# Kernel tuning notes

Hardware: AMD Instinct MI355X
Metric: run time of the kernel (lower is better)

Reference implementation:

```python
import jax, jax.numpy as jnp
import numpy as np

DIM = 1024
ATT_DIM = 1024
BATCH = 16384


def setup_inputs() -> dict:
    key = jax.random.key(0)
    ks = jax.random.split(key, 10)
    inp = {
        "x": jax.random.normal(ks[0], (BATCH, DIM), dtype=jnp.float32),
        "last_x": jax.random.normal(ks[1], (BATCH, DIM), dtype=jnp.float32),
        "last_num": jax.random.normal(ks[2], (BATCH, ATT_DIM), dtype=jnp.float32),
        "last_den": jax.random.uniform(ks[3], (BATCH, ATT_DIM), dtype=jnp.float32) + 1.0,
        # learned parameters
        "mix_k": jnp.full((1, DIM), 0.5, dtype=jnp.float32),
        "mix_v": jnp.full((1, DIM), 0.5, dtype=jnp.float32),
        "mix_r": jnp.full((1, DIM), 0.5, dtype=jnp.float32),
        "decay": jnp.full((1, ATT_DIM), 0.5, dtype=jnp.float32),
        "bonus": jnp.full((1, ATT_DIM), 0.5, dtype=jnp.float32),
        "Wk": jax.random.normal(ks[4], (DIM, ATT_DIM), dtype=jnp.float32) * (DIM ** -0.5),
        "Wv": jax.random.normal(ks[5], (DIM, ATT_DIM), dtype=jnp.float32) * (DIM ** -0.5),
        "Wr": jax.random.normal(ks[6], (DIM, ATT_DIM), dtype=jnp.float32) * (DIM ** -0.5),
        "Wout": jax.random.normal(ks[7], (ATT_DIM, DIM), dtype=jnp.float32) * (ATT_DIM ** -0.5),
    }
    return inp


def reference(x, last_x, last_num, last_den, mix_k, mix_v, mix_r, decay, bonus,
              Wk, Wv, Wr, Wout):
    # interpolated token-shift mixing, then thin projections
    k = (x * mix_k + last_x * (1.0 - mix_k)) @ Wk          # [B, A]
    v = (x * mix_v + last_x * (1.0 - mix_v)) @ Wv          # [B, A]
    r = jax.nn.sigmoid((x * mix_r + last_x * (1.0 - mix_r)) @ Wr)  # [B, A]

    ebk = jnp.exp(bonus + k)                                # [B, A]
    wkv = (last_num + ebk * v) / (last_den + ebk)
    rwkv = r * wkv

    w = jnp.exp(-jnp.exp(decay))                            # [1, A]
    ek = jnp.exp(k)
    num = w * last_num + ek * v
    den = w * last_den + ek

    hidden = rwkv @ Wout                                    # [B, D]
    return (hidden, x, num, den)
```

## Files before the change

### kernel.cpp

```cpp
#include <hip/hip_runtime.h>
#include <stdint.h>


typedef __bf16 bf16;
typedef __bf16 bf16x8 __attribute__((ext_vector_type(8)));
typedef float  f32x4  __attribute__((ext_vector_type(4)));

#define BATCH 16384
#define DIM   1024
#define ADIM  1024
#define FP32_MAGIC 0x3F000000u

__device__ __forceinline__ void loadbf8(const bf16* p, float* d) {
  bf16x8 a = *(const bf16x8*)p;
#pragma unroll
  for (int e = 0; e < 8; ++e) d[e] = (float)a[e];
}
__device__ __forceinline__ void storebf8(bf16* p, const float* d) {
  bf16x8 a;
#pragma unroll
  for (int e = 0; e < 8; ++e) a[e] = (bf16)d[e];
  *(bf16x8*)p = a;
}

template <typename T> struct V8;
template <> struct V8<float> {
  __device__ static void load(const float* p, float* d) {
    f32x4 a = *(const f32x4*)p; f32x4 b = *(const f32x4*)(p + 4);
#pragma unroll
    for (int e = 0; e < 4; ++e) { d[e] = a[e]; d[e + 4] = b[e]; }
  }
  __device__ static void store(float* p, const float* d) {
    f32x4 a, b;
#pragma unroll
    for (int e = 0; e < 4; ++e) { a[e] = d[e]; b[e] = d[e + 4]; }
    *(f32x4*)p = a; *(f32x4*)(p + 4) = b;
  }
};
template <> struct V8<bf16> {
  __device__ static void load(const bf16* p, float* d) { loadbf8(p, d); }
  __device__ static void store(bf16* p, const float* d) { storebf8(p, d); }
};

__device__ __forceinline__ void async_copy16(const bf16* g, bf16* l) {
  __builtin_amdgcn_global_load_lds((const __attribute__((address_space(1))) void*)g,
                                   (__attribute__((address_space(3))) void*)l,
                                   16, 0, 0);
}

template <typename TOut>
__device__ __forceinline__ void gemm_body8(const bf16* __restrict__ A, int lda,
                                           const bf16* __restrict__ BT,
                                           TOut* __restrict__ C,
                                           char* sm, int mtile, int ntile)
{
  constexpr int NT = 16;
  const int tid  = threadIdx.x;
  const int wave = tid >> 6;
  const int lane = tid & 63;
  const int wm = wave >> 2;
  const int wn = wave & 3;
  const long m0 = (long)mtile * 256;
  const long n0 = (long)ntile * 256;

  const int csrc  = (lane & 7) ^ (lane >> 3);
  const int rbase = wave * 16 + (lane >> 3) + ((wave >= 4) ? 64 : 0);
  const int cbase = (wave >> 1) * 64 + (wave & 1) * 16 + (lane >> 3);
  const bf16* pA = A  + (size_t)(m0 + rbase) * lda  + csrc * 8;
  const bf16* pB = BT + (size_t)(n0 + cbase) * 1024 + csrc * 8;
  char* const dA = sm + wave * 2048;
  char* const dB = sm + 32768 + wave * 2048;

  const int fr = lane & 15;
  const int fs = lane >> 4;
  const int c0 = ((fs ^ (fr & 7)) << 4);
  const int c1 = (((fs ^ 4) ^ (fr & 7)) << 4);
  const int raA = (wm * 64 + fr) * 128;
  const int raB = 32768 + (wn * 32 + fr) * 128;

  f32x4 acc[8][4] = {};

#define STAGE_A(tau, u) { \
    char* d_ = dA + (((tau) & 1) << 16) + (u) * 16384; \
    const bf16* s_ = pA + (size_t)((u) * 64) * lda + (size_t)(tau) * 64; \
    async_copy16(s_,           (bf16*)d_); \
    async_copy16(s_ + 8 * lda, (bf16*)(d_ + 1024)); }
#define STAGE_B(tau, u) { \
    char* d_ = dB + (((tau) & 1) << 16) + (u) * 16384; \
    const bf16* s_ = pB + (size_t)((u) * 32) * 1024 + (size_t)(tau) * 64; \
    async_copy16(s_,            (bf16*)d_); \
    async_copy16(s_ + 8 * 1024, (bf16*)(d_ + 1024)); }

  STAGE_B(0, 0); STAGE_A(0, 0); STAGE_A(0, 1); STAGE_B(0, 1);
  STAGE_B(1, 0); STAGE_A(1, 0);
  asm volatile("s_waitcnt vmcnt(4)" ::: "memory");
  __builtin_amdgcn_s_barrier();
  __builtin_amdgcn_sched_barrier(0);

#pragma unroll 2
  for (int t = 0; t < NT; ++t) {
    char* const sb = sm + ((t & 1) << 16);
    bf16x8 a0[4][2], a1[4][2], bq[2][2];

#pragma unroll
    for (int mf = 0; mf < 4; ++mf) {
      a0[mf][0] = *(const bf16x8*)(sb + raA + mf * 2048 + c0);
      a0[mf][1] = *(const bf16x8*)(sb + raA + mf * 2048 + c1);
    }
#pragma unroll
    for (int nf = 0; nf < 2; ++nf) {
      bq[nf][0] = *(const bf16x8*)(sb + raB + nf * 2048 + c0);
      bq[nf][1] = *(const bf16x8*)(sb + raB + nf * 2048 + c1);
    }
    if (t + 1 < NT) STAGE_A(t + 1, 1);
    __builtin_amdgcn_s_barrier();
    asm volatile("s_waitcnt lgkmcnt(0)" ::: "memory");
    __builtin_amdgcn_s_setprio(1);
#pragma unroll
    for (int kk = 0; kk < 2; ++kk)
#pragma unroll
      for (int mf = 0; mf < 4; ++mf)
#pragma unroll
        for (int nf = 0; nf < 2; ++nf)
          acc[mf][nf] = __builtin_amdgcn_mfma_f32_16x16x32_bf16(
              a0[mf][kk], bq[nf][kk], acc[mf][nf], 0, 0, 0);
    __builtin_amdgcn_s_setprio(0);
    __builtin_amdgcn_s_barrier();

#pragma unroll
    for (int mf = 0; mf < 4; ++mf) {
      a1[mf][0] = *(const bf16x8*)(sb + raA + 16384 + mf * 2048 + c0);
      a1[mf][1] = *(const bf16x8*)(sb + raA + 16384 + mf * 2048 + c1);
    }
    if (t + 1 < NT) STAGE_B(t + 1, 1);
    __builtin_amdgcn_s_barrier();
    asm volatile("s_waitcnt lgkmcnt(0)" ::: "memory");
    __builtin_amdgcn_s_setprio(1);
#pragma unroll
    for (int kk = 0; kk < 2; ++kk)
#pragma unroll
      for (int mf = 0; mf < 4; ++mf)
#pragma unroll
        for (int nf = 0; nf < 2; ++nf)
          acc[4 + mf][nf] = __builtin_amdgcn_mfma_f32_16x16x32_bf16(
              a1[mf][kk], bq[nf][kk], acc[4 + mf][nf], 0, 0, 0);
    __builtin_amdgcn_s_setprio(0);
    __builtin_amdgcn_s_barrier();

#pragma unroll
    for (int nf = 0; nf < 2; ++nf) {
      bq[nf][0] = *(const bf16x8*)(sb + raB + 16384 + nf * 2048 + c0);
      bq[nf][1] = *(const bf16x8*)(sb + raB + 16384 + nf * 2048 + c1);
    }
    if (t + 2 < NT) STAGE_B(t + 2, 0);
    __builtin_amdgcn_s_barrier();
    asm volatile("s_waitcnt lgkmcnt(0)" ::: "memory");
    __builtin_amdgcn_s_setprio(1);
#pragma unroll
    for (int kk = 0; kk < 2; ++kk)
#pragma unroll
      for (int mf = 0; mf < 4; ++mf)
#pragma unroll
        for (int nf = 0; nf < 2; ++nf)
          acc[mf][2 + nf] = __builtin_amdgcn_mfma_f32_16x16x32_bf16(
              a0[mf][kk], bq[nf][kk], acc[mf][2 + nf], 0, 0, 0);
    __builtin_amdgcn_s_setprio(0);
    __builtin_amdgcn_s_barrier();

    if (t + 2 < NT) STAGE_A(t + 2, 0);
    __builtin_amdgcn_s_setprio(1);
#pragma unroll
    for (int kk = 0; kk < 2; ++kk)
#pragma unroll
      for (int mf = 0; mf < 4; ++mf)
#pragma unroll
        for (int nf = 0; nf < 2; ++nf)
          acc[4 + mf][2 + nf] = __builtin_amdgcn_mfma_f32_16x16x32_bf16(
              a1[mf][kk], bq[nf][kk], acc[4 + mf][2 + nf], 0, 0, 0);
    __builtin_amdgcn_s_setprio(0);
    if (t < NT - 2)       { asm volatile("s_waitcnt vmcnt(4)" ::: "memory"); }
    else if (t == NT - 2) { asm volatile("s_waitcnt vmcnt(0)" ::: "memory"); }
    __builtin_amdgcn_s_barrier();
    __builtin_amdgcn_sched_barrier(0);
  }
#undef STAGE_A
#undef STAGE_B

  const int cl = fr, rq = fs * 4;
#pragma unroll
  for (int mf = 0; mf < 8; ++mf)
#pragma unroll
    for (int nf = 0; nf < 4; ++nf) {
      const size_t rb = (size_t)(m0 + wm * 128 + mf * 16 + rq) * 1024
                      + (size_t)(n0 + wn * 64 + nf * 16 + cl);
#pragma unroll
      for (int r = 0; r < 4; ++r)
        C[rb + (size_t)r * 1024] = (TOut)acc[mf][nf][r];
    }
}

__device__ __forceinline__ void swz_tiles(int& mtile, int& ntile) {
  const int nbx = gridDim.x, nwg = gridDim.x * gridDim.y;
  int flat = blockIdx.x + blockIdx.y * nbx;
  if ((nwg & 7) == 0 && nwg >= 16) {
    const int cpx = nwg >> 3;
    flat = (flat & 7) * cpx + (flat >> 3);
  }
  ntile = flat % nbx; mtile = flat / nbx;
}

__global__ __launch_bounds__(512, 2) void gemm3_kernel(
    const void* outbase, const bf16* __restrict__ xs,
    const bf16* __restrict__ WkT, const bf16* __restrict__ WvT, const bf16* __restrict__ WrT,
    bf16* kk, bf16* vv, bf16* rp, const uint32_t* probe, long r0)
{
  __shared__ char sm[131072];
  int mtile, ntile; swz_tiles(mtile, ntile);
  const int z = blockIdx.z;
  const bf16* BT = (z == 0) ? WkT : (z == 1) ? WvT : WrT;
  bf16*       Cz = (z == 0) ? kk  : (z == 1) ? vv  : rp;
  const bf16* Az; int lda;
  if (xs) {
    Az  = xs + (size_t)z * BATCH * 1024 + (size_t)r0 * 1024;
    lda = 1024;
  } else {
    const bool f32 = (*probe == FP32_MAGIC);
    const size_t es = f32 ? 4 : 2;
    const size_t reg = (z == 0) ? 0 : (z == 1) ? 2 : 3;
    Az  = (const bf16*)((const char*)outbase + reg * (size_t)BATCH * 1024 * es
                        + (size_t)r0 * 1024 * es);
    lda = (int)(512 * es);
  }
  gemm_body8<bf16>(Az, lda, BT, Cz, sm, mtile, ntile);
}

__global__ __launch_bounds__(512, 2) void gemm1_kernel(
    const bf16* __restrict__ rwkv, const bf16* __restrict__ WoT,
    void* outbase, const uint32_t* probe, long r0)
{
  __shared__ char sm[131072];
  int mtile, ntile; swz_tiles(mtile, ntile);
  if (*probe == FP32_MAGIC)
    gemm_body8<float>(rwkv, 1024, WoT, (float*)outbase + (size_t)r0 * 1024, sm, mtile, ntile);
  else
    gemm_body8<bf16>(rwkv, 1024, WoT, (bf16*)outbase + (size_t)r0 * 1024, sm, mtile, ntile);
}

template <typename T>
__device__ __forceinline__ void transpose_body(const T* W, bf16* WT, float (*t)[33]) {
  const int tx = threadIdx.x & 31, ty = threadIdx.x >> 5;
  const int x0 = blockIdx.x * 32, y0 = blockIdx.y * 32;
#pragma unroll
  for (int i = 0; i < 32; i += 8)
    t[ty + i][tx] = (float)W[(size_t)(y0 + ty + i) * 1024 + x0 + tx];
  __syncthreads();
#pragma unroll
  for (int i = 0; i < 32; i += 8)
    WT[(size_t)(x0 + ty + i) * 1024 + y0 + tx] = (bf16)t[tx][ty + i];
}

__global__ __launch_bounds__(256) void transpose_kernel(const void* W, bf16* WT,
                                                        const uint32_t* probe) {
  __shared__ float t[32][33];
  if (*probe == FP32_MAGIC) transpose_body<float>((const float*)W, WT, t);
  else                      transpose_body<bf16>((const bf16*)W, WT, t);
}

template <typename T>
__device__ __forceinline__ void mix_body(const T* x, const T* lx,
                                         const T* mk, const T* mv, const T* mr,
                                         char* outbase, bf16* xs)
{
  const size_t i8  = ((size_t)blockIdx.x * 256 + threadIdx.x) * 8;
  const size_t row = i8 >> 10;
  const int    col = (int)(i8 & 1023);
  constexpr size_t es = sizeof(T);
  const size_t BDes = (size_t)BATCH * 1024 * es;
  bf16 *xk, *xv, *xr;
  if (xs) {
    const size_t BD = (size_t)BATCH * 1024;
    xk = xs + i8; xv = xs + BD + i8; xr = xs + 2 * BD + i8;
  } else {
    const size_t rowb = row * 1024 * es;
    xk = (bf16*)(outbase + 0 * BDes + rowb) + col;
    xv = (bf16*)(outbase + 2 * BDes + rowb) + col;
    xr = (bf16*)(outbase + 3 * BDes + rowb) + col;
  }
  T* xout = (T*)(outbase + 1 * BDes) + i8;

  float a[8], b[8], k[8], v[8], r[8], ok[8], ov[8], orr[8];
  V8<T>::load(x + i8, a);
  V8<T>::load(lx + i8, b);
  V8<T>::load(mk + col, k);
  V8<T>::load(mv + col, v);
  V8<T>::load(mr + col, r);
#pragma unroll
  for (int e = 0; e < 8; ++e) {
    ok[e]  = a[e] * k[e] + b[e] * (1.0f - k[e]);
    ov[e]  = a[e] * v[e] + b[e] * (1.0f - v[e]);
    orr[e] = a[e] * r[e] + b[e] * (1.0f - r[e]);
  }
  storebf8(xk, ok);
  storebf8(xv, ov);
  storebf8(xr, orr);
  V8<T>::store(xout, a);
}

__global__ __launch_bounds__(256) void mix_kernel(
    const void* x, const void* lx, const void* mk, const void* mv, const void* mr,
    void* outbase, bf16* xs, const uint32_t* probe)
{
  if (*probe == FP32_MAGIC)
    mix_body<float>((const float*)x, (const float*)lx, (const float*)mk,
                    (const float*)mv, (const float*)mr, (char*)outbase, xs);
  else
    mix_body<bf16>((const bf16*)x, (const bf16*)lx, (const bf16*)mk,
                   (const bf16*)mv, (const bf16*)mr, (char*)outbase, xs);
}

template <typename T>
__device__ __forceinline__ void ew2_body(bf16* kk, const bf16* vv, const bf16* rp,
                                         const T* ln, const T* ld,
                                         const T* decay, const T* bonus,
                                         T* numo, T* deno, long grow0)
{
  const size_t li  = ((size_t)blockIdx.x * 256 + threadIdx.x) * 8;
  const size_t gi  = (size_t)grow0 + li;
  const int    col = (int)(gi & (ADIM - 1));
  float k[8], v[8], rr[8], n[8], d[8], de[8], bo[8];
  loadbf8(kk + li, k);
  loadbf8(vv + li, v);
  loadbf8(rp + li, rr);
  V8<T>::load(ln + gi, n);
  V8<T>::load(ld + gi, d);
  V8<T>::load(decay + col, de);
  V8<T>::load(bonus + col, bo);
  float orw[8], onu[8], ode[8];
#pragma unroll
  for (int e = 0; e < 8; ++e) {
    const float r   = 1.0f / (1.0f + __expf(-rr[e]));
    const float ebk = __expf(bo[e] + k[e]);
    const float wkv = (n[e] + ebk * v[e]) / (d[e] + ebk);
    orw[e] = r * wkv;
    const float w  = __expf(-__expf(de[e]));
    const float ek = __expf(k[e]);
    onu[e] = w * n[e] + ek * v[e];
    ode[e] = w * d[e] + ek;
  }
  storebf8(kk + li, orw);
  V8<T>::store(numo + gi, onu);
  V8<T>::store(deno + gi, ode);
}

__global__ __launch_bounds__(256) void ew2_kernel(
    bf16* kk, const bf16* vv, const bf16* rp,
    const void* ln, const void* ld, const void* decay, const void* bonus,
    void* outbase, const uint32_t* probe, long r0)
{
  const long grow0 = r0 * 1024;
  const long BD = (long)BATCH * 1024;
  if (*probe == FP32_MAGIC) {
    float* o = (float*)outbase;
    ew2_body<float>(kk, vv, rp, (const float*)ln, (const float*)ld,
                    (const float*)decay, (const float*)bonus,
                    o + 2 * BD, o + 3 * BD, grow0);
  } else {
    bf16* o = (bf16*)outbase;
    ew2_body<bf16>(kk, vv, rp, (const bf16*)ln, (const bf16*)ld,
                   (const bf16*)decay, (const bf16*)bonus,
                   o + 2 * BD, o + 3 * BD, grow0);
  }
}

extern "C" void kernel_launch(void* const* d_in, const int* in_sizes, int n_in,
                              void* d_out, int out_size, void* d_ws, size_t ws_size,
                              hipStream_t stream)
{
  const void* x     = d_in[0];
  const void* lx    = d_in[1];
  const void* ln    = d_in[2];
  const void* ld    = d_in[3];
  const void* mk    = d_in[4];
  const void* mv    = d_in[5];
  const void* mr    = d_in[6];
  const void* decay = d_in[7];
  const void* bonus = d_in[8];
  const void* Wk    = d_in[9];
  const void* Wv    = d_in[10];
  const void* Wr    = d_in[11];
  const void* Wo    = d_in[12];
  const uint32_t* probe = (const uint32_t*)d_in[4];

  bf16* WkT = (bf16*)d_ws;
  bf16* WvT = WkT + (size_t)DIM * ADIM;
  bf16* WrT = WvT + (size_t)DIM * ADIM;
  bf16* WoT = WrT + (size_t)DIM * ADIM;

  const size_t wt_bytes = 4ull * DIM * ADIM * sizeof(bf16);
  const size_t xs_bytes = 3ull * BATCH * DIM * sizeof(bf16);
  const size_t kv_bytes = 3ull * BATCH * ADIM * sizeof(bf16);

  bf16* xs = nullptr;
  bf16* kk;
  int chunk;
  if (ws_size >= wt_bytes + xs_bytes + kv_bytes) {
    xs = WoT + (size_t)DIM * ADIM;
    kk = xs + 3ull * BATCH * DIM;
    chunk = BATCH;
  } else {
    kk = WoT + (size_t)DIM * ADIM;
    const size_t avail = (ws_size > wt_bytes) ? ws_size - wt_bytes : 0;
    chunk = BATCH;
    while (chunk > 256 && (size_t)chunk * ADIM * sizeof(bf16) * 3 > avail) chunk >>= 1;
  }
  bf16* vv = kk + (size_t)chunk * ADIM;
  bf16* rp = vv + (size_t)chunk * ADIM;

  const dim3 tgrid(32, 32);
  transpose_kernel<<<tgrid, 256, 0, stream>>>(Wk, WkT, probe);
  transpose_kernel<<<tgrid, 256, 0, stream>>>(Wv, WvT, probe);
  transpose_kernel<<<tgrid, 256, 0, stream>>>(Wr, WrT, probe);
  transpose_kernel<<<tgrid, 256, 0, stream>>>(Wo, WoT, probe);

  mix_kernel<<<(size_t)BATCH * DIM / 2048, 256, 0, stream>>>(x, lx, mk, mv, mr,
                                                             d_out, xs, probe);

  for (long r0 = 0; r0 < BATCH; r0 += chunk) {
    const dim3 g3(ADIM / 256, chunk / 256, 3);
    gemm3_kernel<<<g3, 512, 0, stream>>>(d_out, xs, WkT, WvT, WrT, kk, vv, rp, probe, r0);

    ew2_kernel<<<(size_t)chunk * ADIM / 2048, 256, 0, stream>>>(
        kk, vv, rp, ln, ld, decay, bonus, d_out, probe, r0);

    const dim3 g1(DIM / 256, chunk / 256);
    gemm1_kernel<<<g1, 512, 0, stream>>>(kk , WoT, d_out, probe, r0);
  }
}
```

Measured before the change: 646.3 us.

## Restructure GEMM main-loop barriers/prefetch schedule and merge weight transposes into one launch

The GEMM inner loop is reorganized so that the first pair of MFMA groups runs back to back after loading both A halves, with fewer workgroup barriers and lgkmcnt waits per iteration. All of the next-next stage's A halves and one B half are now issued in one batch, so the vmcnt threshold rises from 4 to 6. Separately, the four weight-transpose launches are fused into a single launch using blockIdx.z. The aim is to cut synchronization stalls and launch overhead, at the risk of LDS hazards because buffers are overwritten with fewer barriers and the WkT..WoT buffers are assumed to be contiguous.

```diff
diff --git a/kernel.cpp b/kernel.cpp
--- a/kernel.cpp
+++ b/kernel.cpp
@@ -47,6 +47,8 @@
                                    (__attribute__((address_space(3))) void*)l,
                                    16, 0, 0);
 }
+
+#define SCHED0 __builtin_amdgcn_sched_barrier(0)
 
 template <typename TOut>
 __device__ __forceinline__ void gemm_body8(const bf16* __restrict__ A, int lda,
@@ -91,11 +93,11 @@
     async_copy16(s_,            (bf16*)d_); \
     async_copy16(s_ + 8 * 1024, (bf16*)(d_ + 1024)); }
 
-  STAGE_B(0, 0); STAGE_A(0, 0); STAGE_A(0, 1); STAGE_B(0, 1);
-  STAGE_B(1, 0); STAGE_A(1, 0);
-  asm volatile("s_waitcnt vmcnt(4)" ::: "memory");
+  STAGE_A(0, 0); STAGE_A(0, 1); STAGE_B(0, 0); STAGE_B(0, 1);
+  STAGE_A(1, 0); STAGE_A(1, 1); STAGE_B(1, 0);
+  asm volatile("s_waitcnt vmcnt(6)" ::: "memory");
   __builtin_amdgcn_s_barrier();
-  __builtin_amdgcn_sched_barrier(0);
+  SCHED0;
 
 #pragma unroll 2
   for (int t = 0; t < NT; ++t) {
@@ -112,30 +114,23 @@
       bq[nf][0] = *(const bf16x8*)(sb + raB + nf * 2048 + c0);
       bq[nf][1] = *(const bf16x8*)(sb + raB + nf * 2048 + c1);
     }
-    if (t + 1 < NT) STAGE_A(t + 1, 1);
-    __builtin_amdgcn_s_barrier();
-    asm volatile("s_waitcnt lgkmcnt(0)" ::: "memory");
-    __builtin_amdgcn_s_setprio(1);
-#pragma unroll
-    for (int kk = 0; kk < 2; ++kk)
-#pragma unroll
-      for (int mf = 0; mf < 4; ++mf)
-#pragma unroll
-        for (int nf = 0; nf < 2; ++nf)
-          acc[mf][nf] = __builtin_amdgcn_mfma_f32_16x16x32_bf16(
-              a0[mf][kk], bq[nf][kk], acc[mf][nf], 0, 0, 0);
-    __builtin_amdgcn_s_setprio(0);
-    __builtin_amdgcn_s_barrier();
-
+    SCHED0;
+    if (t + 1 < NT) STAGE_B(t + 1, 1);
 #pragma unroll
     for (int mf = 0; mf < 4; ++mf) {
       a1[mf][0] = *(const bf16x8*)(sb + raA + 16384 + mf * 2048 + c0);
       a1[mf][1] = *(const bf16x8*)(sb + raA + 16384 + mf * 2048 + c1);
     }
-    if (t + 1 < NT) STAGE_B(t + 1, 1);
-    __builtin_amdgcn_s_barrier();
-    asm volatile("s_waitcnt lgkmcnt(0)" ::: "memory");
+    SCHED0;
     __builtin_amdgcn_s_setprio(1);
+#pragma unroll
+    for (int kk = 0; kk < 2; ++kk)
+#pragma unroll
+      for (int mf = 0; mf < 4; ++mf)
+#pragma unroll
+        for (int nf = 0; nf < 2; ++nf)
+          acc[mf][nf] = __builtin_amdgcn_mfma_f32_16x16x32_bf16(
+              a0[mf][kk], bq[nf][kk], acc[mf][nf], 0, 0, 0);
 #pragma unroll
     for (int kk = 0; kk < 2; ++kk)
 #pragma unroll
@@ -146,15 +141,15 @@
               a1[mf][kk], bq[nf][kk], acc[4 + mf][nf], 0, 0, 0);
     __builtin_amdgcn_s_setprio(0);
     __builtin_amdgcn_s_barrier();
-
+    SCHED0;
 #pragma unroll
     for (int nf = 0; nf < 2; ++nf) {
       bq[nf][0] = *(const bf16x8*)(sb + raB + 16384 + nf * 2048 + c0);
       bq[nf][1] = *(const bf16x8*)(sb + raB + 16384 + nf * 2048 + c1);
     }
-    if (t + 2 < NT) STAGE_B(t + 2, 0);
-    __builtin_amdgcn_s_barrier();
-    asm volatile("s_waitcnt lgkmcnt(0)" ::: "memory");
+    SCHED0;
+    if (t + 2 < NT) { STAGE_A(t + 2, 0); STAGE_A(t + 2, 1); STAGE_B(t + 2, 0); }
+    SCHED0;
     __builtin_amdgcn_s_setprio(1);
 #pragma unroll
     for (int kk = 0; kk < 2; ++kk)
@@ -164,11 +159,6 @@
         for (int nf = 0; nf < 2; ++nf)
           acc[mf][2 + nf] = __builtin_amdgcn_mfma_f32_16x16x32_bf16(
               a0[mf][kk], bq[nf][kk], acc[mf][2 + nf], 0, 0, 0);
-    __builtin_amdgcn_s_setprio(0);
-    __builtin_amdgcn_s_barrier();
-
-    if (t + 2 < NT) STAGE_A(t + 2, 0);
-    __builtin_amdgcn_s_setprio(1);
 #pragma unroll
     for (int kk = 0; kk < 2; ++kk)
 #pragma unroll
@@ -178,10 +168,10 @@
           acc[4 + mf][2 + nf] = __builtin_amdgcn_mfma_f32_16x16x32_bf16(
               a1[mf][kk], bq[nf][kk], acc[4 + mf][2 + nf], 0, 0, 0);
     __builtin_amdgcn_s_setprio(0);
-    if (t < NT - 2)       { asm volatile("s_waitcnt vmcnt(4)" ::: "memory"); }
+    if (t < NT - 2)       { asm volatile("s_waitcnt vmcnt(6)" ::: "memory"); }
     else if (t == NT - 2) { asm volatile("s_waitcnt vmcnt(0)" ::: "memory"); }
     __builtin_amdgcn_s_barrier();
-    __builtin_amdgcn_sched_barrier(0);
+    SCHED0;
   }
 #undef STAGE_A
 #undef STAGE_B
@@ -259,9 +249,14 @@
     WT[(size_t)(x0 + ty + i) * 1024 + y0 + tx] = (bf16)t[tx][ty + i];
 }
 
-__global__ __launch_bounds__(256) void transpose_kernel(const void* W, bf16* WT,
-                                                        const uint32_t* probe) {
+__global__ __launch_bounds__(256) void transpose4_kernel(
+    const void* Wk, const void* Wv, const void* Wr, const void* Wo,
+    bf16* WT0, const uint32_t* probe)
+{
   __shared__ float t[32][33];
+  const int z = blockIdx.z;
+  const void* W = (z == 0) ? Wk : (z == 1) ? Wv : (z == 2) ? Wr : Wo;
+  bf16* WT = WT0 + (size_t)z * DIM * ADIM;
   if (*probe == FP32_MAGIC) transpose_body<float>((const float*)W, WT, t);
   else                      transpose_body<bf16>((const bf16*)W, WT, t);
 }
@@ -416,11 +411,7 @@
   bf16* vv = kk + (size_t)chunk * ADIM;
   bf16* rp = vv + (size_t)chunk * ADIM;
 
-  const dim3 tgrid(32, 32);
-  transpose_kernel<<<tgrid, 256, 0, stream>>>(Wk, WkT, probe);
-  transpose_kernel<<<tgrid, 256, 0, stream>>>(Wv, WvT, probe);
-  transpose_kernel<<<tgrid, 256, 0, stream>>>(Wr, WrT, probe);
-  transpose_kernel<<<tgrid, 256, 0, stream>>>(Wo, WoT, probe);
+  transpose4_kernel<<<dim3(32, 32, 4), 256, 0, stream>>>(Wk, Wv, Wr, Wo, WkT, probe);
 
   mix_kernel<<<(size_t)BATCH * DIM / 2048, 256, 0, stream>>>(x, lx, mk, mv, mr,
                                                              d_out, xs, probe);
```

After: 643.3 us. Within noise of the previous version (-0.5%).
